# Optimization experiments

Measured on AMD Instinct MI355X. Metric: run time of the kernel, lower is better.

## Reference

```python
import jax, jax.numpy as jnp
import numpy as np


def setup_inputs() -> dict:
    key = jax.random.key(0)
    k1, k2, k3 = jax.random.split(key, 3)
    B, N, M, S = 2, 8192, 32768, 4096
    pred = jax.random.normal(k1, (B, N, 3), dtype=jnp.float32)
    target = jax.random.normal(k2, (B, M, 3), dtype=jnp.float32)
    # stands in for torch.randperm(N)[:S]; duplicates don't change the math shape-wise
    idx = jax.random.randint(k3, (S,), 0, N, dtype=jnp.int64)
    return {"pred": pred, "target": target, "idx": idx}


def reference(pred, target, idx):
    # pred: (B, N, 3), target: (B, M, 3), idx: (S,)
    pred_s = pred[:, idx, :]                       # (B, S, 3) -- sampled points
    x2 = jnp.sum(pred_s * pred_s, axis=-1)         # (B, S)
    y2 = jnp.sum(target * target, axis=-1)         # (B, M)
    xy = jnp.einsum("bsd,bmd->bsm", pred_s, target)  # (B, S, M)
    d2 = x2[:, :, None] + y2[:, None, :] - 2.0 * xy
    dist = jnp.sqrt(jnp.maximum(d2, 0.0))          # (B, S, M)
    min_dist = jnp.min(dist, axis=2)               # (B, S)
    return jnp.mean(min_dist)
```

## Files before the change

kernel.cpp:

```cpp
#include <hip/hip_runtime.h>
#include <math.h>

typedef float vf2 __attribute__((ext_vector_type(2)));

constexpr int B = 2;
constexpr int N = 8192;
constexpr int M = 32768;
constexpr int S = 4096;
constexpr int QTOT = B * S;
constexpr int R = 16;
constexpr int WT = 64 * R;
constexpr int TCH = M / WT;
constexpr int QG = S / 64;
constexpr int WAVES = B * TCH * QG;
constexpr int BLOCKS = WAVES / 4;


#define DECLP(j) vf2 T0_##j, T1_##j, T2_##j, TY_##j;
#define LOADP(j)                                                         \
  {                                                                      \
    int mA = (2 * j) * 64 + lane, mB = (2 * j + 1) * 64 + lane;          \
    float ax = tb[3 * mA], ay = tb[3 * mA + 1], az = tb[3 * mA + 2];     \
    float bx = tb[3 * mB], by = tb[3 * mB + 1], bz = tb[3 * mB + 2];     \
    T0_##j = vf2{ax, bx};                                                \
    T1_##j = vf2{ay, by};                                                \
    T2_##j = vf2{az, bz};                                                \
    TY_##j = vf2{fmaf(ax, ax, fmaf(ay, ay, az * az)),                    \
                 fmaf(bx, bx, fmaf(by, by, bz * bz))};                   \
  }
#define PAIRC(j, acc)                                                    \
  {                                                                      \
    vf2 s = __builtin_elementwise_fma(Q0, T0_##j, TY_##j);               \
    s = __builtin_elementwise_fma(Q1, T1_##j, s);                        \
    s = __builtin_elementwise_fma(Q2, T2_##j, s);                        \
    acc = fminf(fminf(s.x, s.y), acc);                   \
  }

__global__ __launch_bounds__(256, 4) void chamfer_main(
    const float* __restrict__ pred, const float* __restrict__ target,
    const int* __restrict__ idx, unsigned* __restrict__ wsmin,
    unsigned* __restrict__ ticket, float* __restrict__ out) {
  __shared__ float qs0[64], qs1[64], qs2[64], qw[64];
  __shared__ unsigned qmin[64];
  __shared__ int islast;
  const int lane = threadIdx.x & 63;
  const int w = blockIdx.x * 4 + (threadIdx.x >> 6);
  const int b = w >> 11;
  const int rem = w & 2047;
  const int tch = rem & (TCH - 1);
  const int qg = rem >> 5;

  if (threadIdx.x < 64) {
    int s = qg * 64 + threadIdx.x;
    int i = idx[s];
    const float* p = pred + ((size_t)b * N + (size_t)i) * 3;
    float x = p[0], y = p[1], z = p[2];
    qs0[threadIdx.x] = -2.0f * x;
    qs1[threadIdx.x] = -2.0f * y;
    qs2[threadIdx.x] = -2.0f * z;
    qw[threadIdx.x] = x * x + y * y + z * z;
    qmin[threadIdx.x] = 0xFFFFFFFFu;
  }

  const float* tb = target + ((size_t)b * M + (size_t)tch * WT) * 3;
  DECLP(0) DECLP(1) DECLP(2) DECLP(3) DECLP(4) DECLP(5) DECLP(6) DECLP(7)
  LOADP(0) LOADP(1) LOADP(2) LOADP(3) LOADP(4) LOADP(5) LOADP(6) LOADP(7)
  __syncthreads();

  const float qx2_home = qw[lane];
  const int rot = ((lane + 1) & 63) * 4;
  float mm = INFINITY;
  int qoff = lane;
  float q0 = qs0[qoff], q1 = qs1[qoff], q2 = qs2[qoff];

#pragma unroll 1
  for (int step = 0; step < 64; ++step) {
    int qn = (qoff + 1) & 63;
    float n0 = qs0[qn], n1 = qs1[qn], n2 = qs2[qn];
    vf2 Q0 = vf2{q0, q0}, Q1 = vf2{q1, q1}, Q2 = vf2{q2, q2};
    float m0 = INFINITY, m1 = INFINITY;
    PAIRC(0, m0) PAIRC(1, m1) PAIRC(2, m0) PAIRC(3, m1)
    PAIRC(4, m0) PAIRC(5, m1) PAIRC(6, m0) PAIRC(7, m1)
    mm = fminf(mm, fminf(m0, m1));
    mm = __int_as_float(__builtin_amdgcn_ds_bpermute(rot, __float_as_int(mm)));
    q0 = n0; q1 = n1; q2 = n2; qoff = qn;
  }
  atomicMin(&qmin[lane], __float_as_uint(fmaxf(qx2_home + mm, 0.0f)));
  __syncthreads();

  if (threadIdx.x < 64) {
    int q = b * S + qg * 64 + threadIdx.x;
    atomicMin(&wsmin[q], qmin[threadIdx.x]);
    __threadfence();
  }
  __syncthreads();
  if (threadIdx.x == 0) {
    unsigned t = atomicAdd(ticket, 1u);
    islast = (t == (unsigned)(BLOCKS - 2));
  }
  __syncthreads();
  if (!islast) return;

  float s0 = 0.0f, s1 = 0.0f, s2 = 0.0f, s3 = 0.0f;
#pragma unroll 1
  for (int i = 0; i < QTOT / 256; i += 4) {
    int q = threadIdx.x + i * 256;
    s0 += sqrtf(__uint_as_float(atomicAdd(&wsmin[q], 0u)));
    s1 += sqrtf(__uint_as_float(atomicAdd(&wsmin[q + 256], 0u)));
    s2 += sqrtf(__uint_as_float(atomicAdd(&wsmin[q + 512], 0u)));
    s3 += sqrtf(__uint_as_float(atomicAdd(&wsmin[q + 768], 0u)));
  }
  float sum = (s0 + s1) + (s2 + s3);
#pragma unroll
  for (int off = 32; off > 0; off >>= 1)
    sum += __shfl_down(sum, off, 64);
  __shared__ float red[4];
  int wv = threadIdx.x >> 6;
  if ((threadIdx.x & 63) == 0) red[wv] = sum;
  __syncthreads();
  if (threadIdx.x == 0)
    out[0] = (red[0] + red[1] + red[2] + red[3]) / (float)QTOT;
}

extern "C" void kernel_launch(void* const* d_in, const int* in_sizes, int n_in,
                              void* d_out, int out_size, void* d_ws, size_t ws_size,
                              hipStream_t stream) {
  const float* pred = (const float*)d_in[0];
  const float* target = (const float*)d_in[1];
  const int* idx = (const int*)d_in[2];
  unsigned* wsmin = (unsigned*)d_ws;
  unsigned* ticket = wsmin + QTOT;

  hipMemsetAsync(d_ws, 0xFF, QTOT * sizeof(unsigned) + 4, stream);
  chamfer_main<<<BLOCKS, 256, 0, stream>>>(pred, target, idx, wsmin, ticket,
                                           (float*)d_out);
}
```

Before: 89.55 us.

## Split final reduction into separate kernel and drop block-level LDS min merge

Replaces the last-block ticket scheme (threadfence, global atomic ticket, extra syncthreads) with a second single-block kernel that sums sqrt of the per-query minima. Each wave now does its atomicMin straight to global memory instead of merging the block's four waves in LDS first. This removes the block-wide barriers and fences at the end of the main kernel, at the cost of an extra kernel launch and four times more global atomics.

```diff
diff --git a/kernel.cpp b/kernel.cpp
--- a/kernel.cpp
+++ b/kernel.cpp
@@ -14,7 +14,6 @@
 constexpr int QG = S / 64;
 constexpr int WAVES = B * TCH * QG;
 constexpr int BLOCKS = WAVES / 4;
-
 
 #define DECLP(j) vf2 T0_##j, T1_##j, T2_##j, TY_##j;
 #define LOADP(j)                                                         \
@@ -38,11 +37,8 @@
 
 __global__ __launch_bounds__(256, 4) void chamfer_main(
     const float* __restrict__ pred, const float* __restrict__ target,
-    const int* __restrict__ idx, unsigned* __restrict__ wsmin,
-    unsigned* __restrict__ ticket, float* __restrict__ out) {
+    const int* __restrict__ idx, unsigned* __restrict__ wsmin) {
   __shared__ float qs0[64], qs1[64], qs2[64], qw[64];
-  __shared__ unsigned qmin[64];
-  __shared__ int islast;
   const int lane = threadIdx.x & 63;
   const int w = blockIdx.x * 4 + (threadIdx.x >> 6);
   const int b = w >> 11;
@@ -59,7 +55,6 @@
     qs1[threadIdx.x] = -2.0f * y;
     qs2[threadIdx.x] = -2.0f * z;
     qw[threadIdx.x] = x * x + y * y + z * z;
-    qmin[threadIdx.x] = 0xFFFFFFFFu;
   }
 
   const float* tb = target + ((size_t)b * M + (size_t)tch * WT) * 3;
@@ -85,41 +80,29 @@
     mm = __int_as_float(__builtin_amdgcn_ds_bpermute(rot, __float_as_int(mm)));
     q0 = n0; q1 = n1; q2 = n2; qoff = qn;
   }
-  atomicMin(&qmin[lane], __float_as_uint(fmaxf(qx2_home + mm, 0.0f)));
-  __syncthreads();
+  const int q = b * S + qg * 64 + lane;
+  atomicMin(&wsmin[q], __float_as_uint(fmaxf(qx2_home + mm, 0.0f)));
+}
 
-  if (threadIdx.x < 64) {
-    int q = b * S + qg * 64 + threadIdx.x;
-    atomicMin(&wsmin[q], qmin[threadIdx.x]);
-    __threadfence();
-  }
-  __syncthreads();
-  if (threadIdx.x == 0) {
-    unsigned t = atomicAdd(ticket, 1u);
-    islast = (t == (unsigned)(BLOCKS - 2));
-  }
-  __syncthreads();
-  if (!islast) return;
-
-  float s0 = 0.0f, s1 = 0.0f, s2 = 0.0f, s3 = 0.0f;
-#pragma unroll 1
-  for (int i = 0; i < QTOT / 256; i += 4) {
-    int q = threadIdx.x + i * 256;
-    s0 += sqrtf(__uint_as_float(atomicAdd(&wsmin[q], 0u)));
-    s1 += sqrtf(__uint_as_float(atomicAdd(&wsmin[q + 256], 0u)));
-    s2 += sqrtf(__uint_as_float(atomicAdd(&wsmin[q + 512], 0u)));
-    s3 += sqrtf(__uint_as_float(atomicAdd(&wsmin[q + 768], 0u)));
-  }
-  float sum = (s0 + s1) + (s2 + s3);
+__global__ __launch_bounds__(1024) void chamfer_finish(
+    const unsigned* __restrict__ wsmin, float* __restrict__ out) {
+  __shared__ float red[16];
+  float sum = 0.0f;
+#pragma unroll
+  for (int i = 0; i < QTOT / 1024; ++i)
+    sum += sqrtf(__uint_as_float(wsmin[threadIdx.x + i * 1024]));
 #pragma unroll
   for (int off = 32; off > 0; off >>= 1)
     sum += __shfl_down(sum, off, 64);
-  __shared__ float red[4];
   int wv = threadIdx.x >> 6;
   if ((threadIdx.x & 63) == 0) red[wv] = sum;
   __syncthreads();
-  if (threadIdx.x == 0)
-    out[0] = (red[0] + red[1] + red[2] + red[3]) / (float)QTOT;
+  if (threadIdx.x == 0) {
+    float t = 0.0f;
+#pragma unroll
+    for (int i = 0; i < 16; ++i) t += red[i];
+    out[0] = t / (float)QTOT;
+  }
 }
 
 extern "C" void kernel_launch(void* const* d_in, const int* in_sizes, int n_in,
@@ -129,9 +112,8 @@
   const float* target = (const float*)d_in[1];
   const int* idx = (const int*)d_in[2];
   unsigned* wsmin = (unsigned*)d_ws;
-  unsigned* ticket = wsmin + QTOT;
 
-  hipMemsetAsync(d_ws, 0xFF, QTOT * sizeof(unsigned) + 4, stream);
-  chamfer_main<<<BLOCKS, 256, 0, stream>>>(pred, target, idx, wsmin, ticket,
-                                           (float*)d_out);
+  hipMemsetAsync(wsmin, 0xFF, QTOT * sizeof(unsigned), stream);
+  chamfer_main<<<BLOCKS, 256, 0, stream>>>(pred, target, idx, wsmin);
+  chamfer_finish<<<1, 1024, 0, stream>>>(wsmin, (float*)d_out);
 }
```

After: 83.01 us. 1.08x faster.
